# Kernel optimization log

Hardware: AMD Instinct MI355X
Metric: run time of the kernel (lower is better)

Reference implementation:

```python
import jax, jax.numpy as jnp
import numpy as np

INNER_R = 1.0  # args.r * 0.5
OUTER_R = 2.0  # args.r
AXIS = jnp.array([[0, 0, 1], [0, 0, -1], [0, 1, 0], [0, -1, 0], [1, 0, 0], [-1, 0, 0]],
                 dtype=jnp.float32).T  # (3, 6)


def _cos2(xyz):
    # squared clipped cosine of each point direction vs 6 axes
    norm = jnp.linalg.norm(xyz, axis=-1)               # (B, N)
    cos = jnp.maximum(xyz @ AXIS, 0.0) / (norm[..., None] + 1e-8)
    return cos * cos, norm                              # (B, N, 6), (B, N)


def aggregate(direction, xyz, inner_r, outer_r):
    B, N, D6 = direction.shape
    D = D6 // 6
    cos, norm = _cos2(xyz)
    dw = 1.0 - (norm ** 2 - inner_r ** 2) / (outer_r ** 2 - inner_r ** 2)
    dw = jnp.where(dw < 0, 0.0, dw)
    dw = jnp.where(norm <= 0, 0.0, dw)
    dw = dw / jnp.sum(dw, axis=-1, keepdims=True)       # normalize over N
    cos = cos * dw[..., None]                           # (B, N, 6)
    d = direction.reshape(B, N, D, 6) * cos[:, :, None, :]
    return d.sum(axis=(1, 3))                           # sum over axes then points -> (B, D)


def disperse(signal, xyz):
    B, N, D6 = signal.shape
    D = D6 // 6
    cos, _ = _cos2(xyz)
    return (signal.reshape(B, N, D, 6) * cos[:, :, None, :]).sum(axis=-1)  # (B, N, D)


def batchnorm(x, gamma, beta, eps=1e-5):
    # training-mode BN over leading (sample) dim, biased variance like torch
    m = jnp.mean(x, axis=0)
    v = jnp.var(x, axis=0)
    return (x - m) / jnp.sqrt(v + eps) * gamma + beta


def setup_inputs() -> dict:
    key = jax.random.key(0)
    ks = jax.random.split(key, 10)
    B, N, DIM, ENC, MID, VL = 64, 2048, 10, 256, 64, 128
    s = 0.05
    p = lambda k, sh: jax.random.normal(k, sh, dtype=jnp.float32) * s
    x = jax.random.uniform(ks[0], (B, N, DIM), dtype=jnp.float32)  # xyz in [0,1) keeps points inside outer radius
    return {
        "x": x,
        "Wc": p(ks[1], (ENC, DIM)), "bc": jnp.zeros((ENC,), jnp.float32),
        "Wdir": p(ks[2], (MID * 6, DIM)),
        "g1": jnp.ones((MID,), jnp.float32), "b1": jnp.zeros((MID,), jnp.float32),
        "Wdir2": p(ks[3], (ENC, MID)),
        "g2": jnp.ones((ENC,), jnp.float32), "b2": jnp.zeros((ENC,), jnp.float32),
        "Wf1": p(ks[4], (VL, ENC)), "bf1": jnp.zeros((VL,), jnp.float32),
        "Wcm": p(ks[5], (MID, VL + 3)), "bcm": jnp.zeros((MID,), jnp.float32),
        "Wdc": p(ks[6], (ENC * 6, VL + 3)),
        "Wm0": p(ks[7], (MID, ENC)),
        "g3": jnp.ones((MID,), jnp.float32), "b3": jnp.zeros((MID,), jnp.float32),
        "Wf2": p(ks[8], (DIM - 3, MID)), "bf2": jnp.zeros((DIM - 3,), jnp.float32),
    }


def reference(x, Wc, bc, Wdir, g1, b1, Wdir2, g2, b2, Wf1, bf1,
              Wcm, bcm, Wdc, Wm0, g3, b3, Wf2, bf2):
    B, N, C = x.shape
    xyz = x[:, :, :3]
    points = x[:, :, 3:]

    # ---- GeoConv (encode) ----
    center_in = jnp.concatenate([points[:, 0, :], xyz[:, 0, :]], axis=-1)
    center = center_in @ Wc.T + bc  # computed but unused (matches torch: last_bn applied to direction only)
    dir_in = jnp.concatenate([points, xyz], axis=-1)     # (B, N, C)
    direction = dir_in @ Wdir.T                          # (B, N, mid*6)
    direction = aggregate(direction, xyz, INNER_R, OUTER_R)  # (B, mid)
    direction = jax.nn.relu(batchnorm(direction, g1, b1))
    direction = direction @ Wdir2.T                      # (B, enc_out)
    enc = jax.nn.relu(batchnorm(direction, g2, b2))
    z = enc @ Wf1.T + bf1                                # (B, vector_length)

    # ---- GeoDeConv (decode) ----
    c_in = jnp.concatenate([z, xyz[:, 0, :]], axis=-1)
    center2 = c_in @ Wcm.T + bcm                         # (B, mid)
    VL = z.shape[-1]
    sig = jnp.concatenate([xyz, jnp.broadcast_to(z[:, None, :], (B, N, VL))], axis=-1)
    sig = sig @ Wdc.T                                    # (B, N, enc_out*6)
    sig = disperse(sig, xyz)                             # (B, N, enc_out)
    sig = sig @ Wm0.T                                    # (B, N, mid)
    sig = sig.at[:, 0, :].set(center2)                   # inject center signal
    sig = jax.nn.relu(batchnorm(sig.reshape(B * N, -1), g3, b3)).reshape(B, N, -1)

    y = jax.nn.sigmoid(sig @ Wf2.T + bf2)                # (B, N, dim-3)
    return y
```

## Files before the change

kernel.cpp:

```cpp
#include <hip/hip_runtime.h>
#include <math.h>

#define BATCH 64
#define NPTS  2048
#define OFF_M    0
#define OFF_T2   4096
#define OFF_GP2  5248
#define OFF_V    8192
#define OFF_WF1T 57344
#define OFF_D2P  90112
#define OFF_C2   114688
#define OFF_U2   118784

__global__ __launch_bounds__(256) void k_wa(const float* __restrict__ x,
                                            const float* __restrict__ Wm0,
                                            const float* __restrict__ Wdc,
                                            const float* __restrict__ Wf1,
                                            float* __restrict__ ws) {
    __shared__ __attribute__((aligned(16))) float L[61 * 257];
    int blk = blockIdx.x, t = threadIdx.x;
    if (blk < 24) {
        float* wml = L;
        float* pl  = L + 2112;
        int a = blk >> 2, vq = blk & 3;
        int m = t & 63, vg = t >> 6;
        float acc[8];
#pragma unroll
        for (int i = 0; i < 8; ++i) acc[i] = 0.f;
        for (int e0 = 0; e0 < 256; e0 += 32) {
            for (int g = t; g < 2048; g += 256)
                wml[(g >> 5) * 33 + (g & 31)] = Wm0[(g >> 5) * 256 + e0 + (g & 31)];
            for (int g = t; g < 1024; g += 256)
                pl[(g >> 5) * 36 + (g & 31)] =
                    Wdc[((e0 + (g >> 5)) * 6 + a) * 131 + 3 + vq * 32 + (g & 31)];
            __syncthreads();
#pragma unroll
            for (int e = 0; e < 32; ++e) {
                float wv = wml[m * 33 + e];
                const float4* p4 = (const float4*)(pl + e * 36 + vg * 8);
                float4 pa = p4[0], pb = p4[1];
                acc[0] = fmaf(wv, pa.x, acc[0]); acc[1] = fmaf(wv, pa.y, acc[1]);
                acc[2] = fmaf(wv, pa.z, acc[2]); acc[3] = fmaf(wv, pa.w, acc[3]);
                acc[4] = fmaf(wv, pb.x, acc[4]); acc[5] = fmaf(wv, pb.y, acc[5]);
                acc[6] = fmaf(wv, pb.z, acc[6]); acc[7] = fmaf(wv, pb.w, acc[7]);
            }
            __syncthreads();
        }
#pragma unroll
        for (int vv = 0; vv < 8; ++vv)
            ws[OFF_V + (vq * 32 + vg * 8 + vv) * 384 + m * 6 + a] = acc[vv];
    } else if (blk < 42) {
        float* col = L;
        float* red = L + 256;
        int p = blk - 24, a = p / 3, j = p % 3;
        col[t] = Wdc[(t * 6 + a) * 131 + j];
        __syncthreads();
        int m = t >> 2, q = t & 3;
        const float* wm = Wm0 + m * 256 + q * 64;
        const float* cl = col + q * 64;
        float s = 0.f;
#pragma unroll 8
        for (int i = 0; i < 64; ++i) s = fmaf(wm[i], cl[i], s);
        red[t] = s;
        __syncthreads();
        if (t < 64) {
            float v = (red[t * 4] + red[t * 4 + 1]) + (red[t * 4 + 2] + red[t * 4 + 3]);
            ws[OFF_T2 + t * 18 + a * 3 + j] = v;
        }
    } else if (blk < 106) {
        int b = blk - 42;
        float* red = L;
        float acc[61];
#pragma unroll
        for (int i = 0; i < 61; ++i) acc[i] = 0.f;
#pragma unroll 2
        for (int k = 0; k < 8; ++k) {
            int n = t + 256 * k;
            const float* xp = x + (size_t)(b * NPTS + n) * 10;
            float xv[10];
#pragma unroll
            for (int j = 0; j < 5; ++j) {
                float2 v = *(const float2*)(xp + 2 * j);
                xv[2 * j] = v.x; xv[2 * j + 1] = v.y;
            }
            float x0 = xv[0], x1 = xv[1], x2 = xv[2];
            float rn = x0 * x0 + x1 * x1 + x2 * x2;
            float norm = sqrtf(rn);
            float inv = 1.f / (norm + 1e-8f);
            float c2[6];
            c2[0] = fmaxf(x2, 0.f) * inv; c2[1] = fmaxf(-x2, 0.f) * inv;
            c2[2] = fmaxf(x1, 0.f) * inv; c2[3] = fmaxf(-x1, 0.f) * inv;
            c2[4] = fmaxf(x0, 0.f) * inv; c2[5] = fmaxf(-x0, 0.f) * inv;
#pragma unroll
            for (int a = 0; a < 6; ++a) c2[a] *= c2[a];
            float dw = 1.f - (rn - 1.f) * (1.f / 3.f);
            if (dw < 0.f) dw = 0.f;
            if (norm <= 0.f) dw = 0.f;
            float cw[6];
#pragma unroll
            for (int a = 0; a < 6; ++a) cw[a] = c2[a] * dw;
#pragma unroll
            for (int c = 0; c < 10; ++c) {
                float dv = (c < 7) ? xv[3 + c] : xv[c - 7];
#pragma unroll
                for (int a = 0; a < 6; ++a)
                    acc[c * 6 + a] = fmaf(dv, cw[a], acc[c * 6 + a]);
            }
            acc[60] += dw;
        }
#pragma unroll
        for (int i = 0; i < 61; ++i) red[i * 257 + t] = acc[i];
        __syncthreads();
        if (t < 61) {
            float s = 0.f;
#pragma unroll 8
            for (int j = 0; j < 256; ++j) s += red[t * 257 + j];
            ws[OFF_M + b * 61 + t] = s;
        }
    } else if (blk == 106) {
        for (int g = t; g < 1024; g += 256) ws[OFF_GP2 + g] = 0.f;
    } else {
        float* slab = L;
        int w = blk - 107, v0 = w * 16;
        for (int g = t; g < 4096; g += 256)
            slab[(g >> 8) * 257 + (g & 255)] = Wf1[(v0 + (g >> 8)) * 256 + (g & 255)];
        __syncthreads();
        for (int g = t; g < 4096; g += 256) {
            int e = g >> 4, vl = g & 15;
            ws[OFF_WF1T + e * 128 + v0 + vl] = slab[vl * 257 + e];
        }
    }
}

__global__ __launch_bounds__(256) void k_d2(const float* __restrict__ Wdir,
                                            const float* __restrict__ g1,
                                            const float* __restrict__ b1,
                                            const float* __restrict__ Wdir2,
                                            const float* __restrict__ g2,
                                            const float* __restrict__ b2,
                                            float* __restrict__ ws) {
    __shared__ float L[12704];
    float* Wd  = L;
    float* Ml  = L + 3904;
    float* h1  = L + 7808;
    float* wt2 = L + 11968;
    float* d2l = L + 12228;
    float* sc  = L + 12548;
    float* of  = L + 12612;
    float* scl = L + 12676;
    float* ofl = L + 12680;
    int blk = blockIdx.x, t = threadIdx.x;
    int e_base = blk * 4;
    for (int g = t; g < 64 * 61; g += 256) Ml[g] = ws[OFF_M + g];
    for (int g = t; g < 3840; g += 256) Wd[(g / 60) * 61 + g % 60] = Wdir[g];
    if (t < 256) {
        int el = t >> 6, mm = t & 63;
        wt2[el * 65 + mm] = Wdir2[(e_base + el) * 64 + mm];
    }
    __syncthreads();
    int m = t & 63;
    float Wr[60];
#pragma unroll
    for (int r = 0; r < 60; ++r) Wr[r] = Wd[m * 61 + r];
#pragma unroll
    for (int k = 0; k < 16; ++k) {
        int idx = t + 256 * k;
        int b = idx >> 6;
        const float* Mb = Ml + b * 61;
        float s = 0.f;
#pragma unroll
        for (int a = 0; a < 6; ++a)
#pragma unroll
            for (int c = 0; c < 10; ++c)
                s = fmaf(Wr[a * 10 + c], Mb[c * 6 + a], s);
        h1[b * 65 + m] = s / Mb[60];
    }
    __syncthreads();
    if (t < 64) {
        float s = 0.f, q = 0.f;
#pragma unroll 8
        for (int b = 0; b < 64; ++b) { float v = h1[b * 65 + t]; s += v; q = fmaf(v, v, q); }
        float mean = s * (1.f / 64.f);
        float var = q * (1.f / 64.f) - mean * mean;
        float scale = g1[t] * rsqrtf(var + 1e-5f);
        sc[t] = scale; of[t] = b1[t] - mean * scale;
    }
    __syncthreads();
#pragma unroll
    for (int k = 0; k < 16; ++k) {
        int idx = t + 256 * k;
        int b = idx >> 6;
        h1[b * 65 + m] = fmaxf(fmaf(h1[b * 65 + m], sc[m], of[m]), 0.f);
    }
    __syncthreads();
    {
        int b = t >> 2, el = t & 3;
        const float* h = h1 + b * 65;
        const float* w = wt2 + el * 65;
        float s = 0.f;
#pragma unroll
        for (int mm = 0; mm < 64; ++mm) s = fmaf(h[mm], w[mm], s);
        d2l[b * 5 + el] = s;
    }
    __syncthreads();
    if (t < 4) {
        float s = 0.f, q = 0.f;
#pragma unroll 8
        for (int b = 0; b < 64; ++b) { float v = d2l[b * 5 + t]; s += v; q = fmaf(v, v, q); }
        float mean = s * (1.f / 64.f);
        float var = q * (1.f / 64.f) - mean * mean;
        int E = e_base + t;
        float scale = g2[E] * rsqrtf(var + 1e-5f);
        scl[t] = scale; ofl[t] = b2[E] - mean * scale;
    }
    __syncthreads();
    {
        int b = t >> 2, el = t & 3;
        float v = fmaxf(fmaf(d2l[b * 5 + el], scl[el], ofl[el]), 0.f);
        ws[OFF_D2P + b * 256 + e_base + el] = v;
    }
}

__global__ __launch_bounds__(512) void k_c(const float* __restrict__ x,
                                           const float* __restrict__ bf1,
                                           const float* __restrict__ Wcm,
                                           const float* __restrict__ bcm,
                                           float* __restrict__ ws) {
    __shared__ float L[13120];
    float* xl    = L;
    float* zl    = L + 1024;
    float* T2l   = L + 1152;
    float* U2l   = L + 2304;
    float* r2    = L + 2688;
    float* d2row = L + 3712;
    float* zp    = L + 3968;
    float* wl    = L + 4480;
    float* C2l   = L + 12992;
    float* h0l   = L + 13056;
    int blk = blockIdx.x, t = threadIdx.x;
    int b = blk >> 3, c = blk & 7;
    const float* xb = x + (size_t)b * NPTS * 10;
    if (t < 256) {
        const float* xp = xb + (size_t)(c * 256 + t) * 10;
        float2 v01 = *(const float2*)xp;
        xl[t * 4 + 0] = v01.x; xl[t * 4 + 1] = v01.y; xl[t * 4 + 2] = xp[2];
        d2row[t] = ws[OFF_D2P + b * 256 + t];
    }
    for (int g = t; g < 1152; g += 512) T2l[g] = ws[OFF_T2 + g];
    if (c == 0)
        for (int g = t; g < 8384; g += 512) wl[(g / 131) * 133 + g % 131] = Wcm[g];
    __syncthreads();
    {
        int q = t >> 7, v = t & 127;
        const float* Wt = ws + OFF_WF1T + (q * 64) * 128 + v;
        const float* d = d2row + q * 64;
        float s = 0.f;
#pragma unroll 8
        for (int e = 0; e < 64; ++e) s = fmaf(d[e], Wt[e * 128], s);
        zp[q * 128 + v] = s;
    }
    __syncthreads();
    if (t < 128)
        zl[t] = bf1[t] + ((zp[t] + zp[128 + t]) + (zp[256 + t] + zp[384 + t]));
    __syncthreads();
    if (t < 384) {
        const float* Vt = ws + OFF_V;
        float s0 = 0.f;
#pragma unroll 8
        for (int v = 0; v < 128; ++v) s0 = fmaf(zl[v], Vt[v * 384 + t], s0);
        U2l[t] = s0;
        if (c == 0) ws[OFF_U2 + b * 384 + t] = s0;
    } else if (c == 0 && t < 448) {
        int m = t - 384;
        const float* w = wl + m * 133;
        float s = bcm[m];
#pragma unroll 4
        for (int i = 0; i < 128; ++i) s = fmaf(zl[i], w[i], s);
        s = fmaf(xl[0], w[128], s);
        s = fmaf(xl[1], w[129], s);
        s = fmaf(xl[2], w[130], s);
        ws[OFF_C2 + b * 64 + m] = s;
        C2l[m] = s;
    }
    __syncthreads();
    int m = t & 63;
    int g = __builtin_amdgcn_readfirstlane(t >> 6);
    float T[18], U[6];
#pragma unroll
    for (int r = 0; r < 18; ++r) T[r] = T2l[m * 18 + r];
#pragma unroll
    for (int a = 0; a < 6; ++a) U[a] = U2l[m * 6 + a];
    float accS = 0.f, accQ = 0.f;
    const float* xw = xl + g * 32 * 4;
#pragma unroll 4
    for (int i = 0; i < 32; ++i) {
        float x0 = xw[i * 4], x1 = xw[i * 4 + 1], x2 = xw[i * 4 + 2];
        float rn = x0 * x0 + x1 * x1 + x2 * x2;
        float inv = 1.f / (sqrtf(rn) + 1e-8f);
        float c2[6];
        c2[0] = fmaxf(x2, 0.f) * inv; c2[1] = fmaxf(-x2, 0.f) * inv;
        c2[2] = fmaxf(x1, 0.f) * inv; c2[3] = fmaxf(-x1, 0.f) * inv;
        c2[4] = fmaxf(x0, 0.f) * inv; c2[5] = fmaxf(-x0, 0.f) * inv;
        float h = 0.f;
#pragma unroll
        for (int a = 0; a < 6; ++a) {
            float cc = c2[a] * c2[a];
            float ta = fmaf(x0, T[a * 3], fmaf(x1, T[a * 3 + 1], fmaf(x2, T[a * 3 + 2], U[a])));
            h = fmaf(cc, ta, h);
        }
        if (c == 0 && g == 0 && i == 0) h0l[m] = h;
        accS += h;
        accQ = fmaf(h, h, accQ);
    }
    r2[t] = accS; r2[512 + t] = accQ;
    __syncthreads();
    if (t < 64) {
        float s = 0.f;
#pragma unroll
        for (int gg = 0; gg < 8; ++gg) s += r2[gg * 64 + t];
        if (c == 0) s += C2l[t] - h0l[t];
        atomicAdd(&ws[OFF_GP2 + c * 128 + t], s);
    } else if (t < 128) {
        int mm = t - 64;
        float q = 0.f;
#pragma unroll
        for (int gg = 0; gg < 8; ++gg) q += r2[512 + gg * 64 + mm];
        if (c == 0) q += C2l[mm] * C2l[mm] - h0l[mm] * h0l[mm];
        atomicAdd(&ws[OFF_GP2 + c * 128 + t], q);
    }
}

__global__ __launch_bounds__(512) void k_e(const float* __restrict__ x,
                                           const float* __restrict__ g3,
                                           const float* __restrict__ b3,
                                           const float* __restrict__ Wf2,
                                           const float* __restrict__ bf2,
                                           const float* __restrict__ ws,
                                           float* __restrict__ out) {
    __shared__ __attribute__((aligned(16))) float L[6464];
    float* Wl24 = L;
    float* Pl   = L + 1536;
    float* C2l  = L + 2304;
    float* yp   = L + 2368;
    int blk = blockIdx.x, t = threadIdx.x;
    int b = blk >> 3;
    for (int g = t; g < 1152; g += 512) {
        int m = g / 18, r = g % 18, a = r / 3, j = r % 3;
        Wl24[m * 24 + a * 4 + j] = ws[OFF_T2 + g];
    }
    if (t < 384)
        Wl24[(t / 6) * 24 + (t % 6) * 4 + 3] = ws[OFF_U2 + b * 384 + t];
    if (t < 448) {
        int m = t / 7, k = t % 7;
        Pl[m * 12 + k] = Wf2[k * 64 + m];
    }
    if (t < 64) {
        float S = 0.f, Q = 0.f;
#pragma unroll
        for (int r = 0; r < 8; ++r) {
            S += ws[OFF_GP2 + r * 128 + t];
            Q += ws[OFF_GP2 + r * 128 + 64 + t];
        }
        float mean = S * (1.f / 131072.f);
        float var = Q * (1.f / 131072.f) - mean * mean;
        float scale = g3[t] * rsqrtf(var + 1e-5f);
        Pl[t * 12 + 7] = scale;
        Pl[t * 12 + 8] = b3[t] - mean * scale;
    }
    if ((blk & 7) == 0 && t < 64) C2l[t] = ws[OFF_C2 + b * 64 + t];
    __syncthreads();

    int p_loc = t >> 1, mh = t & 1;
    int p = blk * 256 + p_loc;
    const float* xp = x + (size_t)p * 10;
    float x0 = xp[0], x1 = xp[1], x2 = xp[2];
    float rn = x0 * x0 + x1 * x1 + x2 * x2;
    float inv = 1.f / (sqrtf(rn) + 1e-8f);
    float c2[6];
    c2[0] = fmaxf(x2, 0.f) * inv; c2[1] = fmaxf(-x2, 0.f) * inv;
    c2[2] = fmaxf(x1, 0.f) * inv; c2[3] = fmaxf(-x1, 0.f) * inv;
    c2[4] = fmaxf(x0, 0.f) * inv; c2[5] = fmaxf(-x0, 0.f) * inv;
#pragma unroll
    for (int a = 0; a < 6; ++a) c2[a] *= c2[a];
    bool c0 = ((p & 2047) == 0);
    float y[7];
#pragma unroll
    for (int k = 0; k < 7; ++k) y[k] = mh ? 0.f : bf2[k];
    int m0 = mh * 32;
#pragma unroll 4
    for (int mm = 0; mm < 32; ++mm) {
        int m = m0 + mm;
        const float4* Wm = (const float4*)(Wl24 + m * 24);
        float h = 0.f;
#pragma unroll
        for (int a = 0; a < 6; ++a) {
            float4 wq = Wm[a];
            float ta = fmaf(x0, wq.x, fmaf(x1, wq.y, fmaf(x2, wq.z, wq.w)));
            h = fmaf(c2[a], ta, h);
        }
        if (c0) h = C2l[m];
        const float4* Pm = (const float4*)(Pl + m * 12);
        float4 p0 = Pm[0], p1 = Pm[1];
        float offv = Pl[m * 12 + 8];
        float r = fmaxf(fmaf(h, p1.w, offv), 0.f);
        y[0] = fmaf(r, p0.x, y[0]); y[1] = fmaf(r, p0.y, y[1]);
        y[2] = fmaf(r, p0.z, y[2]); y[3] = fmaf(r, p0.w, y[3]);
        y[4] = fmaf(r, p1.x, y[4]); y[5] = fmaf(r, p1.y, y[5]);
        y[6] = fmaf(r, p1.z, y[6]);
    }
#pragma unroll
    for (int k = 0; k < 7; ++k) yp[p_loc * 16 + mh * 8 + k] = y[k];
    __syncthreads();
    float* op = out + (size_t)blk * 1792;
    for (int g = t; g < 1792; g += 512) {
        int pp = g / 7, k = g % 7;
        float v = yp[pp * 16 + k] + yp[pp * 16 + 8 + k];
        op[g] = 1.f / (1.f + __expf(-v));
    }
}

extern "C" void kernel_launch(void* const* d_in, const int* in_sizes, int n_in,
                              void* d_out, int out_size, void* d_ws, size_t ws_size,
                              hipStream_t stream) {
    const float* x     = (const float*)d_in[0];
    const float* Wdir  = (const float*)d_in[3];
    const float* g1    = (const float*)d_in[4];
    const float* b1    = (const float*)d_in[5];
    const float* Wdir2 = (const float*)d_in[6];
    const float* g2    = (const float*)d_in[7];
    const float* b2    = (const float*)d_in[8];
    const float* Wf1   = (const float*)d_in[9];
    const float* bf1   = (const float*)d_in[10];
    const float* Wcm   = (const float*)d_in[11];
    const float* bcm   = (const float*)d_in[12];
    const float* Wdc   = (const float*)d_in[13];
    const float* Wm0   = (const float*)d_in[14];
    const float* g3    = (const float*)d_in[15];
    const float* b3    = (const float*)d_in[16];
    const float* Wf2   = (const float*)d_in[17];
    const float* bf2   = (const float*)d_in[18];
    float* ws  = (float*)d_ws;
    float* out = (float*)d_out;

    k_wa <<<115, 256, 0, stream>>>(x, Wm0, Wdc, Wf1, ws);
    k_d2 <<<64,  256, 0, stream>>>(Wdir, g1, b1, Wdir2, g2, b2, ws);
    k_c  <<<512, 512, 0, stream>>>(x, bf1, Wcm, bcm, ws);
    k_e  <<<512, 512, 0, stream>>>(x, g3, b3, Wf2, bf2, ws, out);
}
```

Baseline: 179.2 us.

## Compute BN3 statistics from precomputed per-batch xyz moments instead of per-point pass

The decoder batchnorm statistics (sum and sum of squares of the pre-BN signal) are rewritten algebraically. Per-batch moment tensors of cos² and xyz (up to second order in xyz and in cos² products) are accumulated in extra k_wa blocks. The old k_c, which re-evaluated h for every point in 512 blocks, becomes k_z with 64 blocks that contract those moments with T and U. This removes a full per-point pass, but adds heavy register use (126 accumulators) in the new k_wa blocks and a different floating-point summation order.

```diff
diff --git a/kernel.cpp b/kernel.cpp
--- a/kernel.cpp
+++ b/kernel.cpp
@@ -11,6 +11,7 @@
 #define OFF_D2P  90112
 #define OFF_C2   114688
 #define OFF_U2   118784
+#define OFF_MOM  143360
 
 __global__ __launch_bounds__(256) void k_wa(const float* __restrict__ x,
                                             const float* __restrict__ Wm0,
@@ -118,8 +119,8 @@
             ws[OFF_M + b * 61 + t] = s;
         }
     } else if (blk == 106) {
-        for (int g = t; g < 1024; g += 256) ws[OFF_GP2 + g] = 0.f;
-    } else {
+        if (t < 128) ws[OFF_GP2 + t] = 0.f;
+    } else if (blk < 115) {
         float* slab = L;
         int w = blk - 107, v0 = w * 16;
         for (int g = t; g < 4096; g += 256)
@@ -128,6 +129,121 @@
         for (int g = t; g < 4096; g += 256) {
             int e = g >> 4, vl = g & 15;
             ws[OFF_WF1T + e * 128 + v0 + vl] = slab[vl * 257 + e];
+        }
+    } else if (blk < 179) {
+        int b = blk - 115;
+        float* red = L;
+        float acc[126];
+#pragma unroll
+        for (int i = 0; i < 126; ++i) acc[i] = 0.f;
+        for (int k = 0; k < 8; ++k) {
+            int n = t + 256 * k;
+            const float* xp = x + (size_t)(b * NPTS + n) * 10;
+            float x0 = xp[0], x1 = xp[1], x2 = xp[2];
+            float rn = x0 * x0 + x1 * x1 + x2 * x2;
+            float inv = 1.f / (sqrtf(rn) + 1e-8f);
+            float c[6];
+            c[0] = fmaxf(x2, 0.f) * inv; c[1] = fmaxf(-x2, 0.f) * inv;
+            c[2] = fmaxf(x1, 0.f) * inv; c[3] = fmaxf(-x1, 0.f) * inv;
+            c[4] = fmaxf(x0, 0.f) * inv; c[5] = fmaxf(-x0, 0.f) * inv;
+#pragma unroll
+            for (int a = 0; a < 6; ++a) c[a] *= c[a];
+            float xx[6] = {x0 * x0, x0 * x1, x0 * x2, x1 * x1, x1 * x2, x2 * x2};
+#pragma unroll
+            for (int a = 0; a < 6; ++a)
+#pragma unroll
+                for (int a2 = a; a2 < 6; ++a2) {
+                    int p = a * 6 - (a * (a - 1)) / 2 + (a2 - a);
+                    float cc = c[a] * c[a2];
+#pragma unroll
+                    for (int q = 0; q < 6; ++q)
+                        acc[p * 6 + q] = fmaf(cc, xx[q], acc[p * 6 + q]);
+                }
+        }
+#pragma unroll
+        for (int i = 0; i < 61; ++i) red[i * 257 + t] = acc[i];
+        __syncthreads();
+        if (t < 61) {
+            float s = 0.f;
+#pragma unroll 8
+            for (int j = 0; j < 256; ++j) s += red[t * 257 + j];
+            ws[OFF_MOM + b * 240 + 108 + t] = s;
+        }
+        __syncthreads();
+#pragma unroll
+        for (int i = 0; i < 61; ++i) red[i * 257 + t] = acc[61 + i];
+        __syncthreads();
+        if (t < 61) {
+            float s = 0.f;
+#pragma unroll 8
+            for (int j = 0; j < 256; ++j) s += red[t * 257 + j];
+            ws[OFF_MOM + b * 240 + 108 + 61 + t] = s;
+        }
+        __syncthreads();
+#pragma unroll
+        for (int i = 0; i < 4; ++i) red[i * 257 + t] = acc[122 + i];
+        __syncthreads();
+        if (t < 4) {
+            float s = 0.f;
+#pragma unroll 8
+            for (int j = 0; j < 256; ++j) s += red[t * 257 + j];
+            ws[OFF_MOM + b * 240 + 108 + 122 + t] = s;
+        }
+    } else {
+        int b = blk - 179;
+        float* red = L;
+        float acc[108];
+#pragma unroll
+        for (int i = 0; i < 108; ++i) acc[i] = 0.f;
+        for (int k = 0; k < 8; ++k) {
+            int n = t + 256 * k;
+            const float* xp = x + (size_t)(b * NPTS + n) * 10;
+            float x0 = xp[0], x1 = xp[1], x2 = xp[2];
+            float rn = x0 * x0 + x1 * x1 + x2 * x2;
+            float inv = 1.f / (sqrtf(rn) + 1e-8f);
+            float c[6];
+            c[0] = fmaxf(x2, 0.f) * inv; c[1] = fmaxf(-x2, 0.f) * inv;
+            c[2] = fmaxf(x1, 0.f) * inv; c[3] = fmaxf(-x1, 0.f) * inv;
+            c[4] = fmaxf(x0, 0.f) * inv; c[5] = fmaxf(-x0, 0.f) * inv;
+#pragma unroll
+            for (int a = 0; a < 6; ++a) c[a] *= c[a];
+#pragma unroll
+            for (int a = 0; a < 6; ++a) {
+                acc[a] += c[a];
+                acc[6 + a * 3 + 0] = fmaf(c[a], x0, acc[6 + a * 3 + 0]);
+                acc[6 + a * 3 + 1] = fmaf(c[a], x1, acc[6 + a * 3 + 1]);
+                acc[6 + a * 3 + 2] = fmaf(c[a], x2, acc[6 + a * 3 + 2]);
+            }
+#pragma unroll
+            for (int a = 0; a < 6; ++a)
+#pragma unroll
+                for (int a2 = a; a2 < 6; ++a2) {
+                    int p = a * 6 - (a * (a - 1)) / 2 + (a2 - a);
+                    float cc = c[a] * c[a2];
+                    acc[24 + p] += cc;
+                    acc[45 + p * 3 + 0] = fmaf(cc, x0, acc[45 + p * 3 + 0]);
+                    acc[45 + p * 3 + 1] = fmaf(cc, x1, acc[45 + p * 3 + 1]);
+                    acc[45 + p * 3 + 2] = fmaf(cc, x2, acc[45 + p * 3 + 2]);
+                }
+        }
+#pragma unroll
+        for (int i = 0; i < 61; ++i) red[i * 257 + t] = acc[i];
+        __syncthreads();
+        if (t < 61) {
+            float s = 0.f;
+#pragma unroll 8
+            for (int j = 0; j < 256; ++j) s += red[t * 257 + j];
+            ws[OFF_MOM + b * 240 + t] = s;
+        }
+        __syncthreads();
+#pragma unroll
+        for (int i = 0; i < 47; ++i) red[i * 257 + t] = acc[61 + i];
+        __syncthreads();
+        if (t < 47) {
+            float s = 0.f;
+#pragma unroll 8
+            for (int j = 0; j < 256; ++j) s += red[t * 257 + j];
+            ws[OFF_MOM + b * 240 + 61 + t] = s;
         }
     }
 }
@@ -221,34 +337,27 @@
     }
 }
 
-__global__ __launch_bounds__(512) void k_c(const float* __restrict__ x,
+__global__ __launch_bounds__(512) void k_z(const float* __restrict__ x,
                                            const float* __restrict__ bf1,
                                            const float* __restrict__ Wcm,
                                            const float* __restrict__ bcm,
                                            float* __restrict__ ws) {
-    __shared__ float L[13120];
-    float* xl    = L;
-    float* zl    = L + 1024;
-    float* T2l   = L + 1152;
-    float* U2l   = L + 2304;
-    float* r2    = L + 2688;
-    float* d2row = L + 3712;
-    float* zp    = L + 3968;
-    float* wl    = L + 4480;
-    float* C2l   = L + 12992;
-    float* h0l   = L + 13056;
-    int blk = blockIdx.x, t = threadIdx.x;
-    int b = blk >> 3, c = blk & 7;
-    const float* xb = x + (size_t)b * NPTS * 10;
-    if (t < 256) {
-        const float* xp = xb + (size_t)(c * 256 + t) * 10;
-        float2 v01 = *(const float2*)xp;
-        xl[t * 4 + 0] = v01.x; xl[t * 4 + 1] = v01.y; xl[t * 4 + 2] = xp[2];
-        d2row[t] = ws[OFF_D2P + b * 256 + t];
-    }
+    __shared__ float L[11252];
+    float* d2row = L;
+    float* T2l   = L + 256;
+    float* zp    = L + 1408;
+    float* zl    = L + 1920;
+    float* U2l   = L + 2048;
+    float* C2l   = L + 2432;
+    float* mom   = L + 2496;
+    float* x0l   = L + 2736;
+    float* wl    = L + 2740;
+    int b = blockIdx.x, t = threadIdx.x;
+    if (t < 256) d2row[t] = ws[OFF_D2P + b * 256 + t];
     for (int g = t; g < 1152; g += 512) T2l[g] = ws[OFF_T2 + g];
-    if (c == 0)
-        for (int g = t; g < 8384; g += 512) wl[(g / 131) * 133 + g % 131] = Wcm[g];
+    if (t < 234) mom[t] = ws[OFF_MOM + b * 240 + t];
+    if (t < 3) x0l[t] = x[(size_t)b * NPTS * 10 + t];
+    for (int g = t; g < 8384; g += 512) wl[(g / 131) * 133 + g % 131] = Wcm[g];
     __syncthreads();
     {
         int q = t >> 7, v = t & 127;
@@ -269,64 +378,75 @@
 #pragma unroll 8
         for (int v = 0; v < 128; ++v) s0 = fmaf(zl[v], Vt[v * 384 + t], s0);
         U2l[t] = s0;
-        if (c == 0) ws[OFF_U2 + b * 384 + t] = s0;
-    } else if (c == 0 && t < 448) {
+        ws[OFF_U2 + b * 384 + t] = s0;
+    } else if (t < 448) {
         int m = t - 384;
         const float* w = wl + m * 133;
         float s = bcm[m];
 #pragma unroll 4
         for (int i = 0; i < 128; ++i) s = fmaf(zl[i], w[i], s);
-        s = fmaf(xl[0], w[128], s);
-        s = fmaf(xl[1], w[129], s);
-        s = fmaf(xl[2], w[130], s);
+        s = fmaf(x0l[0], w[128], s);
+        s = fmaf(x0l[1], w[129], s);
+        s = fmaf(x0l[2], w[130], s);
         ws[OFF_C2 + b * 64 + m] = s;
         C2l[m] = s;
     }
     __syncthreads();
-    int m = t & 63;
-    int g = __builtin_amdgcn_readfirstlane(t >> 6);
-    float T[18], U[6];
-#pragma unroll
-    for (int r = 0; r < 18; ++r) T[r] = T2l[m * 18 + r];
-#pragma unroll
-    for (int a = 0; a < 6; ++a) U[a] = U2l[m * 6 + a];
-    float accS = 0.f, accQ = 0.f;
-    const float* xw = xl + g * 32 * 4;
-#pragma unroll 4
-    for (int i = 0; i < 32; ++i) {
-        float x0 = xw[i * 4], x1 = xw[i * 4 + 1], x2 = xw[i * 4 + 2];
-        float rn = x0 * x0 + x1 * x1 + x2 * x2;
+    if (t < 64) {
+        int m = t;
+        float T[18], U[6];
+#pragma unroll
+        for (int r = 0; r < 18; ++r) T[r] = T2l[m * 18 + r];
+#pragma unroll
+        for (int a = 0; a < 6; ++a) U[a] = U2l[m * 6 + a];
+        float S = 0.f;
+#pragma unroll
+        for (int a = 0; a < 6; ++a) {
+            S = fmaf(mom[6 + a * 3 + 0], T[a * 3 + 0], S);
+            S = fmaf(mom[6 + a * 3 + 1], T[a * 3 + 1], S);
+            S = fmaf(mom[6 + a * 3 + 2], T[a * 3 + 2], S);
+            S = fmaf(mom[a], U[a], S);
+        }
+        float qd = 0.f, qo = 0.f;
+#pragma unroll
+        for (int a = 0; a < 6; ++a)
+#pragma unroll
+            for (int a2 = a; a2 < 6; ++a2) {
+                int p = a * 6 - (a * (a - 1)) / 2 + (a2 - a);
+                const float* b3 = mom + 108 + p * 6;
+                const float* b2 = mom + 45 + p * 3;
+                float b1v = mom[24 + p];
+                float Ta0 = T[a * 3], Ta1 = T[a * 3 + 1], Ta2 = T[a * 3 + 2];
+                float Tb0 = T[a2 * 3], Tb1 = T[a2 * 3 + 1], Tb2 = T[a2 * 3 + 2];
+                float w0 = b3[0] * Ta0 + b3[1] * Ta1 + b3[2] * Ta2;
+                float w1 = b3[1] * Ta0 + b3[3] * Ta1 + b3[4] * Ta2;
+                float w2 = b3[2] * Ta0 + b3[4] * Ta1 + b3[5] * Ta2;
+                float term = w0 * Tb0 + w1 * Tb1 + w2 * Tb2;
+                float d1 = b2[0] * Ta0 + b2[1] * Ta1 + b2[2] * Ta2;
+                float d2_ = b2[0] * Tb0 + b2[1] * Tb1 + b2[2] * Tb2;
+                term += U[a2] * d1 + U[a] * d2_ + U[a] * U[a2] * b1v;
+                if (a == a2) qd += term; else qo += term;
+            }
+        float Q = qd + 2.f * qo;
+        float xx0 = x0l[0], xx1 = x0l[1], xx2 = x0l[2];
+        float rn = xx0 * xx0 + xx1 * xx1 + xx2 * xx2;
         float inv = 1.f / (sqrtf(rn) + 1e-8f);
         float c2[6];
-        c2[0] = fmaxf(x2, 0.f) * inv; c2[1] = fmaxf(-x2, 0.f) * inv;
-        c2[2] = fmaxf(x1, 0.f) * inv; c2[3] = fmaxf(-x1, 0.f) * inv;
-        c2[4] = fmaxf(x0, 0.f) * inv; c2[5] = fmaxf(-x0, 0.f) * inv;
-        float h = 0.f;
+        c2[0] = fmaxf(xx2, 0.f) * inv; c2[1] = fmaxf(-xx2, 0.f) * inv;
+        c2[2] = fmaxf(xx1, 0.f) * inv; c2[3] = fmaxf(-xx1, 0.f) * inv;
+        c2[4] = fmaxf(xx0, 0.f) * inv; c2[5] = fmaxf(-xx0, 0.f) * inv;
+        float h0 = 0.f;
 #pragma unroll
         for (int a = 0; a < 6; ++a) {
             float cc = c2[a] * c2[a];
-            float ta = fmaf(x0, T[a * 3], fmaf(x1, T[a * 3 + 1], fmaf(x2, T[a * 3 + 2], U[a])));
-            h = fmaf(cc, ta, h);
-        }
-        if (c == 0 && g == 0 && i == 0) h0l[m] = h;
-        accS += h;
-        accQ = fmaf(h, h, accQ);
-    }
-    r2[t] = accS; r2[512 + t] = accQ;
-    __syncthreads();
-    if (t < 64) {
-        float s = 0.f;
-#pragma unroll
-        for (int gg = 0; gg < 8; ++gg) s += r2[gg * 64 + t];
-        if (c == 0) s += C2l[t] - h0l[t];
-        atomicAdd(&ws[OFF_GP2 + c * 128 + t], s);
-    } else if (t < 128) {
-        int mm = t - 64;
-        float q = 0.f;
-#pragma unroll
-        for (int gg = 0; gg < 8; ++gg) q += r2[512 + gg * 64 + mm];
-        if (c == 0) q += C2l[mm] * C2l[mm] - h0l[mm] * h0l[mm];
-        atomicAdd(&ws[OFF_GP2 + c * 128 + t], q);
+            float ta = fmaf(xx0, T[a * 3], fmaf(xx1, T[a * 3 + 1], fmaf(xx2, T[a * 3 + 2], U[a])));
+            h0 = fmaf(cc, ta, h0);
+        }
+        float C2v = C2l[m];
+        S += C2v - h0;
+        Q += C2v * C2v - h0 * h0;
+        atomicAdd(&ws[OFF_GP2 + m], S);
+        atomicAdd(&ws[OFF_GP2 + 64 + m], Q);
     }
 }
 
@@ -355,12 +475,8 @@
         Pl[m * 12 + k] = Wf2[k * 64 + m];
     }
     if (t < 64) {
-        float S = 0.f, Q = 0.f;
-#pragma unroll
-        for (int r = 0; r < 8; ++r) {
-            S += ws[OFF_GP2 + r * 128 + t];
-            Q += ws[OFF_GP2 + r * 128 + 64 + t];
-        }
+        float S = ws[OFF_GP2 + t];
+        float Q = ws[OFF_GP2 + 64 + t];
         float mean = S * (1.f / 131072.f);
         float var = Q * (1.f / 131072.f) - mean * mean;
         float scale = g3[t] * rsqrtf(var + 1e-5f);
@@ -442,8 +558,8 @@
     float* ws  = (float*)d_ws;
     float* out = (float*)d_out;
 
-    k_wa <<<115, 256, 0, stream>>>(x, Wm0, Wdc, Wf1, ws);
+    k_wa <<<243, 256, 0, stream>>>(x, Wm0, Wdc, Wf1, ws);
     k_d2 <<<64,  256, 0, stream>>>(Wdir, g1, b1, Wdir2, g2, b2, ws);
-    k_c  <<<512, 512, 0, stream>>>(x, bf1, Wcm, bcm, ws);
+    k_z  <<<64,  512, 0, stream>>>(x, bf1, Wcm, bcm, ws);
     k_e  <<<512, 512, 0, stream>>>(x, g3, b3, Wf2, bf2, ws, out);
 }
```

New measurement: 165.5 us. 1.08x faster.
